# Kernel tuning notes

Measured on AMD Instinct MI355X. Metric: run time of the kernel, lower is better.

## Reference

```python
import jax, jax.numpy as jnp
import numpy as np

DIM = 512
EPS = 1e-8
LN_EPS = 1e-5


def _layernorm(x, g, b):
    mu = jnp.mean(x, axis=-1, keepdims=True)
    var = jnp.mean(jnp.square(x - mu), axis=-1, keepdims=True)
    return (x - mu) * jax.lax.rsqrt(var + LN_EPS) * g + b


def setup_inputs() -> dict:
    key = jax.random.key(0)
    ks = jax.random.split(key, 8)
    b, i, j, d = 8, 2048, 2048, DIM
    s = 1.0 / np.sqrt(d)
    return {
        "inputs": jax.random.normal(ks[0], (b, i, d), dtype=jnp.float32),
        "context": jax.random.normal(ks[1], (b, j, d), dtype=jnp.float32),
        "g_in": jnp.ones((d,), jnp.float32),
        "b_in": jnp.zeros((d,), jnp.float32),
        "g_ctx": jnp.ones((d,), jnp.float32),
        "b_ctx": jnp.zeros((d,), jnp.float32),
        "Wq": jax.random.uniform(ks[2], (d, d), jnp.float32, -s, s),
        "bq": jnp.zeros((d,), jnp.float32),
        "Wk": jax.random.uniform(ks[3], (d, d), jnp.float32, -s, s),
        "bk": jnp.zeros((d,), jnp.float32),
        "Wv": jax.random.uniform(ks[4], (d, d), jnp.float32, -s, s),
        "bv": jnp.zeros((d,), jnp.float32),
    }


def reference(inputs, context, g_in, b_in, g_ctx, b_ctx, Wq, bq, Wk, bk, Wv, bv):
    scale = DIM ** (-0.5)
    x = _layernorm(inputs, g_in, b_in)
    c = _layernorm(context, g_ctx, b_ctx)
    q = x @ Wq + bq          # [b,i,d]
    k = c @ Wk + bk          # [b,j,d]
    v = c @ Wv + bv          # [b,j,d]
    dots = jnp.einsum('bid,bjd->bij', q, k) * scale
    # NOTE: non-standard softmax over the QUERY axis (dim=1), then eps shift
    attn = jax.nn.softmax(dots, axis=1) + EPS
    # second renormalization over the KEY axis (dim=2)
    mean_attn = attn / (jnp.sum(attn, axis=2, keepdims=True) + EPS)
    updates = jnp.einsum('bjd,bij->bid', v, mean_attn)
    return updates
```

## Files before the change

kernel.cpp:

```cpp
#include <hip/hip_runtime.h>
#include <hip/hip_bf16.h>
#include <math.h>

#define EPSF 1e-8f
#define LN_EPSF 1e-5f
#define SCALE_QK 0.04419417382415922f

typedef unsigned short ushort_t;
typedef __bf16 bhalf;
typedef bhalf bhalf8 __attribute__((ext_vector_type(8)));
typedef float f32x4 __attribute__((ext_vector_type(4)));

__device__ __forceinline__ float b2f(ushort_t u) {
    return __uint_as_float((unsigned)u << 16);
}
__device__ __forceinline__ ushort_t f2b(float f) {
    unsigned x = __float_as_uint(f);
    return (ushort_t)((x + 0x7fffu + ((x >> 16) & 1u)) >> 16);
}
__device__ __forceinline__ unsigned mulpack2(unsigned u, float ca, float cb) {
    float lo = b2f((ushort_t)(u & 0xffffu)) * ca;
    float hi = b2f((ushort_t)(u >> 16)) * cb;
    return (unsigned)f2b(lo) | ((unsigned)f2b(hi) << 16);
}
__device__ __forceinline__ uint4 scale8(uint4 a, float4 c0, float4 c1) {
    a.x = mulpack2(a.x, c0.x, c0.y);
    a.y = mulpack2(a.y, c0.z, c0.w);
    a.z = mulpack2(a.z, c1.x, c1.y);
    a.w = mulpack2(a.w, c1.z, c1.w);
    return a;
}

__global__ __launch_bounds__(256) void ln_apply_kernel(
    const float* __restrict__ X1, const float* __restrict__ X2,
    const float* __restrict__ g1, const float* __restrict__ b1,
    const float* __restrict__ g2, const float* __restrict__ b2,
    ushort_t* __restrict__ O1, ushort_t* __restrict__ O2)
{
    const bool sec = blockIdx.y != 0;
    const float* X = sec ? X2 : X1;
    const float* g = sec ? g2 : g1;
    const float* b = sec ? b2 : b1;
    ushort_t* O = sec ? O2 : O1;
    const size_t base = (size_t)blockIdx.x * 512;
    const int t = threadIdx.x;
    float a = X[base + t];
    float c = X[base + t + 256];
    float s = a + c;
    float q = fmaf(a, a, c * c);
#pragma unroll
    for (int off = 32; off > 0; off >>= 1) {
        s += __shfl_down(s, off, 64);
        q += __shfl_down(q, off, 64);
    }
    __shared__ float ls[4], lq[4], mv[2];
    int lane = t & 63, w = t >> 6;
    if (lane == 0) { ls[w] = s; lq[w] = q; }
    __syncthreads();
    if (t == 0) {
        float st = ls[0] + ls[1] + ls[2] + ls[3];
        float qt = lq[0] + lq[1] + lq[2] + lq[3];
        float mu = st * (1.0f / 512.0f);
        float var = qt * (1.0f / 512.0f) - mu * mu;
        mv[0] = mu;
        mv[1] = rsqrtf(var + LN_EPSF);
    }
    __syncthreads();
    float mu = mv[0], rstd = mv[1];
    O[base + t]       = f2b((a - mu) * rstd * g[t] + b[t]);
    O[base + t + 256] = f2b((c - mu) * rstd * g[t + 256] + b[t + 256]);
}

__global__ __launch_bounds__(256) void wtrans_kernel(
    const float* __restrict__ W0, const float* __restrict__ W1,
    const float* __restrict__ W2,
    ushort_t* __restrict__ T0, ushort_t* __restrict__ T1,
    ushort_t* __restrict__ T2)
{
    const float* W = blockIdx.z == 0 ? W0 : (blockIdx.z == 1 ? W1 : W2);
    ushort_t* T = blockIdx.z == 0 ? T0 : (blockIdx.z == 1 ? T1 : T2);
    __shared__ float tile[32][33];
    int tx = threadIdx.x & 31, ty = threadIdx.x >> 5;
    int r0 = blockIdx.y * 32, c0 = blockIdx.x * 32;
#pragma unroll
    for (int p = 0; p < 4; ++p)
        tile[ty + p * 8][tx] = W[(size_t)(r0 + ty + p * 8) * 512 + c0 + tx];
    __syncthreads();
#pragma unroll
    for (int p = 0; p < 4; ++p)
        T[(size_t)(c0 + ty + p * 8) * 512 + r0 + tx] = f2b(tile[tx][ty + p * 8]);
}

__global__ __launch_bounds__(256) void vtrans_kernel(
    const ushort_t* __restrict__ V, ushort_t* __restrict__ VT)
{
    __shared__ ushort_t tile[32][33];
    const size_t vb = (size_t)blockIdx.z * 2048 * 512;
    const size_t tb = (size_t)blockIdx.z * 512 * 2048;
    int tx = threadIdx.x & 31, ty = threadIdx.x >> 5;
    int j0 = blockIdx.y * 32, d0 = blockIdx.x * 32;
#pragma unroll
    for (int p = 0; p < 4; ++p)
        tile[ty + p * 8][tx] = V[vb + (size_t)(j0 + ty + p * 8) * 512 + d0 + tx];
    __syncthreads();
#pragma unroll
    for (int p = 0; p < 4; ++p)
        VT[tb + (size_t)(d0 + ty + p * 8) * 2048 + j0 + tx] = tile[tx][ty + p * 8];
}

template <int MODE>
__global__ __launch_bounds__(256) void mfma_gemm_kernel(
    const ushort_t* __restrict__ A, const ushort_t* __restrict__ B,
    void* __restrict__ Cout, const float* __restrict__ aux,
    float* __restrict__ colsum, const float* __restrict__ colrecip,
    int K, int N, size_t strideA, size_t strideB, size_t strideC,
    int auxStride, float scale)
{
    __shared__ ushort_t As[128][40];
    __shared__ ushort_t Bs[128][40];
    const int tid = threadIdx.x;
    const ushort_t* Ab = A + strideA * blockIdx.z;
    const ushort_t* Bb = B + strideB * blockIdx.z;
    const int m0 = blockIdx.y * 128;
    const int n0 = blockIdx.x * 128;
    const int sr = tid >> 2;
    const int sc = (tid & 3) * 8;
    const int wave = tid >> 6;
    const int lane = tid & 63;
    const int fm = lane & 15;
    const int fq = lane >> 4;
    const int wm = (wave >> 1) * 64;
    const int wn = (wave & 1) * 64;

    f32x4 acc[4][4];
#pragma unroll
    for (int i = 0; i < 4; ++i)
#pragma unroll
        for (int j = 0; j < 4; ++j) acc[i][j] = (f32x4){0.f, 0.f, 0.f, 0.f};

    const ushort_t* Arow0 = Ab + (size_t)(m0 + sr) * K + sc;
    const ushort_t* Arow1 = Ab + (size_t)(m0 + sr + 64) * K + sc;
    const ushort_t* Brow0 = Bb + (size_t)(n0 + sr) * K + sc;
    const ushort_t* Brow1 = Bb + (size_t)(n0 + sr + 64) * K + sc;

    for (int k0 = 0; k0 < K; k0 += 32) {
        uint4 a0 = *(const uint4*)(Arow0 + k0);
        uint4 a1 = *(const uint4*)(Arow1 + k0);
        uint4 b0 = *(const uint4*)(Brow0 + k0);
        uint4 b1 = *(const uint4*)(Brow1 + k0);
        if (MODE == 2) {
            const float* cr = colrecip + 2048 * blockIdx.z + k0 + sc;
            float4 c0 = *(const float4*)cr;
            float4 c1 = *(const float4*)(cr + 4);
            a0 = scale8(a0, c0, c1);
            a1 = scale8(a1, c0, c1);
        }
        __syncthreads();
        *(uint4*)&As[sr][sc] = a0;
        *(uint4*)&As[sr + 64][sc] = a1;
        *(uint4*)&Bs[sr][sc] = b0;
        *(uint4*)&Bs[sr + 64][sc] = b1;
        __syncthreads();
        bhalf8 af[4], bfr[4];
#pragma unroll
        for (int t = 0; t < 4; ++t) {
            af[t]  = *(const bhalf8*)&As[wm + t * 16 + fm][fq * 8];
            bfr[t] = *(const bhalf8*)&Bs[wn + t * 16 + fm][fq * 8];
        }
#pragma unroll
        for (int i = 0; i < 4; ++i)
#pragma unroll
            for (int j = 0; j < 4; ++j)
                acc[i][j] = __builtin_amdgcn_mfma_f32_16x16x32_bf16(
                    af[i], bfr[j], acc[i][j], 0, 0, 0);
    }

    if (MODE == 2) {
        float* C = (float*)Cout + strideC * blockIdx.z;
        const float* rc = aux + (size_t)auxStride * blockIdx.z;
#pragma unroll
        for (int ti = 0; ti < 4; ++ti) {
#pragma unroll
            for (int r = 0; r < 4; ++r) {
                int row = m0 + wm + ti * 16 + fq * 4 + r;
                float rs = rc[row];
#pragma unroll
                for (int tj = 0; tj < 4; ++tj) {
                    int col = n0 + wn + tj * 16 + fm;
                    C[(size_t)row * N + col] = acc[ti][tj][r] * rs;
                }
            }
        }
    } else if (MODE == 1) {
        ushort_t* C = (ushort_t*)Cout + strideC * blockIdx.z;
        float* colpart = (float*)&As[0][0];
        __syncthreads();
        if (tid < 128) colpart[tid] = 0.f;
        __syncthreads();
        float psum[4] = {0.f, 0.f, 0.f, 0.f};
#pragma unroll
        for (int ti = 0; ti < 4; ++ti) {
#pragma unroll
            for (int r = 0; r < 4; ++r) {
                int row = m0 + wm + ti * 16 + fq * 4 + r;
#pragma unroll
                for (int tj = 0; tj < 4; ++tj) {
                    int col = n0 + wn + tj * 16 + fm;
                    float e = __expf(acc[ti][tj][r] * scale);
                    ushort_t h = f2b(e);
                    C[(size_t)row * N + col] = h;
                    psum[tj] += b2f(h);
                }
            }
        }
#pragma unroll
        for (int tj = 0; tj < 4; ++tj)
            atomicAdd(&colpart[wn + tj * 16 + fm], psum[tj]);
        __syncthreads();
        if (tid < 128)
            atomicAdd(&colsum[2048 * blockIdx.z + n0 + tid], colpart[tid]);
    } else {
        ushort_t* C = (ushort_t*)Cout + strideC * blockIdx.z;
#pragma unroll
        for (int ti = 0; ti < 4; ++ti) {
#pragma unroll
            for (int r = 0; r < 4; ++r) {
                int row = m0 + wm + ti * 16 + fq * 4 + r;
#pragma unroll
                for (int tj = 0; tj < 4; ++tj) {
                    int col = n0 + wn + tj * 16 + fm;
                    C[(size_t)row * N + col] = f2b(acc[ti][tj][r] + aux[col]);
                }
            }
        }
    }
}

__global__ __launch_bounds__(256) void colrecip_kernel(
    const float* __restrict__ cs, float* __restrict__ cr)
{
    int t = blockIdx.x * 256 + threadIdx.x;
    cr[t] = 1.0f / cs[t];
}

__global__ __launch_bounds__(256) void rowsum_kernel(
    const ushort_t* __restrict__ E, const float* __restrict__ colrecip,
    float* __restrict__ recip)
{
    const uint4* rp = (const uint4*)(E + (size_t)blockIdx.x * 2048);
    const float4* cr = (const float4*)(colrecip + (blockIdx.x >> 11) * 2048);
    uint4 u = rp[threadIdx.x];
    float4 c0 = cr[threadIdx.x * 2];
    float4 c1 = cr[threadIdx.x * 2 + 1];
    float s = b2f((ushort_t)(u.x & 0xffffu)) * c0.x
            + b2f((ushort_t)(u.x >> 16))    * c0.y
            + b2f((ushort_t)(u.y & 0xffffu)) * c0.z
            + b2f((ushort_t)(u.y >> 16))    * c0.w
            + b2f((ushort_t)(u.z & 0xffffu)) * c1.x
            + b2f((ushort_t)(u.z >> 16))    * c1.y
            + b2f((ushort_t)(u.w & 0xffffu)) * c1.z
            + b2f((ushort_t)(u.w >> 16))    * c1.w;
#pragma unroll
    for (int off = 32; off > 0; off >>= 1) s += __shfl_down(s, off, 64);
    __shared__ float ls[4];
    int lane = threadIdx.x & 63, wv = threadIdx.x >> 6;
    if (lane == 0) ls[wv] = s;
    __syncthreads();
    if (threadIdx.x == 0)
        recip[blockIdx.x] = 1.0f / (ls[0] + ls[1] + ls[2] + ls[3] + 2.049e-5f);
}

extern "C" void kernel_launch(void* const* d_in, const int* in_sizes, int n_in,
                              void* d_out, int out_size, void* d_ws, size_t ws_size,
                              hipStream_t stream)
{
    const float* inputs  = (const float*)d_in[0];
    const float* context = (const float*)d_in[1];
    const float* g_in    = (const float*)d_in[2];
    const float* b_in    = (const float*)d_in[3];
    const float* g_ctx   = (const float*)d_in[4];
    const float* b_ctx   = (const float*)d_in[5];
    const float* Wq      = (const float*)d_in[6];
    const float* bq      = (const float*)d_in[7];
    const float* Wk      = (const float*)d_in[8];
    const float* bk      = (const float*)d_in[9];
    const float* Wv      = (const float*)d_in[10];
    const float* bv      = (const float*)d_in[11];
    float* out = (float*)d_out;

    const size_t QKV  = 8ull * 2048 * 512;
    const size_t WSZ  = 512ull * 512;
    const size_t DOTS = 8ull * 2048 * 2048;

    ushort_t* xln   = (ushort_t*)d_ws;
    ushort_t* cln   = xln + QKV;
    ushort_t* WqT   = cln + QKV;
    ushort_t* WkT   = WqT + WSZ;
    ushort_t* WvT   = WkT + WSZ;
    ushort_t* q     = WvT + WSZ;
    ushort_t* kk    = q + QKV;
    ushort_t* v     = kk + QKV;
    ushort_t* vT    = v + QKV;
    ushort_t* edots = vT + QKV;
    float* recip    = (float*)(edots + DOTS);
    float* colsum   = recip + 16384;
    float* colrecip = colsum + 16384;
    size_t need_bytes = (6 * QKV + 3 * WSZ + DOTS) * 2 + 3 * 16384 * 4;
    if (ws_size < need_bytes) return;

    hipMemsetAsync(colsum, 0, 16384 * sizeof(float), stream);

    ln_apply_kernel<<<dim3(16384, 2), 256, 0, stream>>>(
        inputs, context, g_in, b_in, g_ctx, b_ctx, xln, cln);

    wtrans_kernel<<<dim3(16, 16, 3), 256, 0, stream>>>(Wq, Wk, Wv, WqT, WkT, WvT);

    mfma_gemm_kernel<0><<<dim3(4, 128, 1), 256, 0, stream>>>(
        xln, WqT, q, bq, nullptr, nullptr, 512, 512, 0, 0, 0, 0, 1.f);
    mfma_gemm_kernel<0><<<dim3(4, 128, 1), 256, 0, stream>>>(
        cln, WkT, kk, bk, nullptr, nullptr, 512, 512, 0, 0, 0, 0, 1.f);
    mfma_gemm_kernel<0><<<dim3(4, 128, 1), 256, 0, stream>>>(
        cln, WvT, v, bv, nullptr, nullptr, 512, 512, 0, 0, 0, 0, 1.f);

    vtrans_kernel<<<dim3(16, 64, 8), 256, 0, stream>>>(v, vT);

    mfma_gemm_kernel<1><<<dim3(16, 16, 8), 256, 0, stream>>>(
        q, kk, edots, nullptr, colsum, nullptr, 512, 2048,
        (size_t)2048 * 512, (size_t)2048 * 512, (size_t)2048 * 2048, 0, SCALE_QK);

    colrecip_kernel<<<64, 256, 0, stream>>>(colsum, colrecip);
    rowsum_kernel<<<16384, 256, 0, stream>>>(edots, colrecip, recip);

    mfma_gemm_kernel<2><<<dim3(4, 16, 8), 256, 0, stream>>>(
        edots, vT, out, recip, nullptr, colrecip, 2048, 512,
        (size_t)2048 * 2048, (size_t)512 * 2048, (size_t)2048 * 512, 2048, 1.f);
}
```

Measured before the change: 367.8 us.

## Use direct global-to-LDS loads with XOR swizzle and fold colrecip into V transpose

The GEMM main loop now fetches A/B tiles with global_load_lds straight into an XOR-swizzled LDS layout. The K step grows from 32 to 64, which halves the number of barriers. The per-column softmax reciprocal is moved out of the final GEMM's A-operand load and applied once when V is transposed. The column-sum epilogue reduces across lanes with shuffles before the LDS atomics. Together these aim to remove register staging, bank conflicts and repeated scaling work, at the cost of extra bf16 rounding on the scaled V instead of the scaled exp values.

```diff
diff --git a/kernel.cpp b/kernel.cpp
--- a/kernel.cpp
+++ b/kernel.cpp
@@ -18,17 +18,10 @@
     unsigned x = __float_as_uint(f);
     return (ushort_t)((x + 0x7fffu + ((x >> 16) & 1u)) >> 16);
 }
-__device__ __forceinline__ unsigned mulpack2(unsigned u, float ca, float cb) {
-    float lo = b2f((ushort_t)(u & 0xffffu)) * ca;
-    float hi = b2f((ushort_t)(u >> 16)) * cb;
-    return (unsigned)f2b(lo) | ((unsigned)f2b(hi) << 16);
-}
-__device__ __forceinline__ uint4 scale8(uint4 a, float4 c0, float4 c1) {
-    a.x = mulpack2(a.x, c0.x, c0.y);
-    a.y = mulpack2(a.y, c0.z, c0.w);
-    a.z = mulpack2(a.z, c1.x, c1.y);
-    a.w = mulpack2(a.w, c1.z, c1.w);
-    return a;
+__device__ __forceinline__ void gload16(const ushort_t* g, ushort_t* l) {
+    __builtin_amdgcn_global_load_lds(
+        (const __attribute__((address_space(1))) unsigned int*)g,
+        (__attribute__((address_space(3))) unsigned int*)l, 16, 0, 0);
 }
 
 __global__ __launch_bounds__(256) void ln_apply_kernel(
@@ -91,8 +84,9 @@
         T[(size_t)(c0 + ty + p * 8) * 512 + r0 + tx] = f2b(tile[tx][ty + p * 8]);
 }
 
-__global__ __launch_bounds__(256) void vtrans_kernel(
-    const ushort_t* __restrict__ V, ushort_t* __restrict__ VT)
+__global__ __launch_bounds__(256) void vtrans_scaled_kernel(
+    const ushort_t* __restrict__ V, const float* __restrict__ colrecip,
+    ushort_t* __restrict__ VT)
 {
     __shared__ ushort_t tile[32][33];
     const size_t vb = (size_t)blockIdx.z * 2048 * 512;
@@ -102,77 +96,90 @@
 #pragma unroll
     for (int p = 0; p < 4; ++p)
         tile[ty + p * 8][tx] = V[vb + (size_t)(j0 + ty + p * 8) * 512 + d0 + tx];
+    float cr = colrecip[blockIdx.z * 2048 + j0 + tx];
     __syncthreads();
 #pragma unroll
     for (int p = 0; p < 4; ++p)
-        VT[tb + (size_t)(d0 + ty + p * 8) * 2048 + j0 + tx] = tile[tx][ty + p * 8];
+        VT[tb + (size_t)(d0 + ty + p * 8) * 2048 + j0 + tx] =
+            f2b(b2f(tile[tx][ty + p * 8]) * cr);
 }
 
 template <int MODE>
 __global__ __launch_bounds__(256) void mfma_gemm_kernel(
     const ushort_t* __restrict__ A, const ushort_t* __restrict__ B,
     void* __restrict__ Cout, const float* __restrict__ aux,
-    float* __restrict__ colsum, const float* __restrict__ colrecip,
+    float* __restrict__ colsum,
     int K, int N, size_t strideA, size_t strideB, size_t strideC,
     int auxStride, float scale)
 {
-    __shared__ ushort_t As[128][40];
-    __shared__ ushort_t Bs[128][40];
+    __shared__ __align__(16) ushort_t As[128 * 64];
+    __shared__ __align__(16) ushort_t Bs[128 * 64];
     const int tid = threadIdx.x;
     const ushort_t* Ab = A + strideA * blockIdx.z;
     const ushort_t* Bb = B + strideB * blockIdx.z;
     const int m0 = blockIdx.y * 128;
     const int n0 = blockIdx.x * 128;
-    const int sr = tid >> 2;
-    const int sc = (tid & 3) * 8;
     const int wave = tid >> 6;
     const int lane = tid & 63;
     const int fm = lane & 15;
     const int fq = lane >> 4;
+    const int fm7 = fm & 7;
     const int wm = (wave >> 1) * 64;
     const int wn = (wave & 1) * 64;
 
+    const int lrow = lane >> 3;
+    const int lchunk = lane & 7;
+    const int scs = lchunk ^ lrow;
+
+    const ushort_t* aSrc[4]; const ushort_t* bSrc[4];
+    ushort_t* aDst[4]; ushort_t* bDst[4];
+#pragma unroll
+    for (int p = 0; p < 4; ++p) {
+        int row = wave * 32 + p * 8 + lrow;
+        aSrc[p] = Ab + (size_t)(m0 + row) * K + scs * 8;
+        bSrc[p] = Bb + (size_t)(n0 + row) * K + scs * 8;
+        aDst[p] = As + (wave * 32 + p * 8) * 64 + lane * 8;
+        bDst[p] = Bs + (wave * 32 + p * 8) * 64 + lane * 8;
+    }
+
+    const int cBase = fq ^ fm7;
+    const ushort_t* aFrag[4]; const ushort_t* bFrag[4];
+#pragma unroll
+    for (int t = 0; t < 4; ++t) {
+        aFrag[t] = As + (wm + t * 16 + fm) * 64;
+        bFrag[t] = Bs + (wn + t * 16 + fm) * 64;
+    }
+
     f32x4 acc[4][4];
 #pragma unroll
     for (int i = 0; i < 4; ++i)
 #pragma unroll
         for (int j = 0; j < 4; ++j) acc[i][j] = (f32x4){0.f, 0.f, 0.f, 0.f};
 
-    const ushort_t* Arow0 = Ab + (size_t)(m0 + sr) * K + sc;
-    const ushort_t* Arow1 = Ab + (size_t)(m0 + sr + 64) * K + sc;
-    const ushort_t* Brow0 = Bb + (size_t)(n0 + sr) * K + sc;
-    const ushort_t* Brow1 = Bb + (size_t)(n0 + sr + 64) * K + sc;
-
-    for (int k0 = 0; k0 < K; k0 += 32) {
-        uint4 a0 = *(const uint4*)(Arow0 + k0);
-        uint4 a1 = *(const uint4*)(Arow1 + k0);
-        uint4 b0 = *(const uint4*)(Brow0 + k0);
-        uint4 b1 = *(const uint4*)(Brow1 + k0);
-        if (MODE == 2) {
-            const float* cr = colrecip + 2048 * blockIdx.z + k0 + sc;
-            float4 c0 = *(const float4*)cr;
-            float4 c1 = *(const float4*)(cr + 4);
-            a0 = scale8(a0, c0, c1);
-            a1 = scale8(a1, c0, c1);
-        }
-        __syncthreads();
-        *(uint4*)&As[sr][sc] = a0;
-        *(uint4*)&As[sr + 64][sc] = a1;
-        *(uint4*)&Bs[sr][sc] = b0;
-        *(uint4*)&Bs[sr + 64][sc] = b1;
-        __syncthreads();
-        bhalf8 af[4], bfr[4];
-#pragma unroll
-        for (int t = 0; t < 4; ++t) {
-            af[t]  = *(const bhalf8*)&As[wm + t * 16 + fm][fq * 8];
-            bfr[t] = *(const bhalf8*)&Bs[wn + t * 16 + fm][fq * 8];
-        }
-#pragma unroll
-        for (int i = 0; i < 4; ++i)
-#pragma unroll
-            for (int j = 0; j < 4; ++j)
-                acc[i][j] = __builtin_amdgcn_mfma_f32_16x16x32_bf16(
-                    af[i], bfr[j], acc[i][j], 0, 0, 0);
+    for (int k0 = 0; k0 < K; k0 += 64) {
+        __syncthreads();
+#pragma unroll
+        for (int p = 0; p < 4; ++p) {
+            gload16(aSrc[p] + k0, aDst[p]);
+            gload16(bSrc[p] + k0, bDst[p]);
+        }
+        __syncthreads();
+#pragma unroll
+        for (int s = 0; s < 2; ++s) {
+            const int off = ((cBase ^ (s << 2)) << 3);
+            bhalf8 af[4], bf[4];
+#pragma unroll
+            for (int t = 0; t < 4; ++t) {
+                af[t] = *(const bhalf8*)(aFrag[t] + off);
+                bf[t] = *(const bhalf8*)(bFrag[t] + off);
+            }
+#pragma unroll
+            for (int i = 0; i < 4; ++i)
+#pragma unroll
+                for (int j = 0; j < 4; ++j)
+                    acc[i][j] = __builtin_amdgcn_mfma_f32_16x16x32_bf16(
+                        af[i], bf[j], acc[i][j], 0, 0, 0);
+        }
     }
 
     if (MODE == 2) {
@@ -193,10 +200,7 @@
         }
     } else if (MODE == 1) {
         ushort_t* C = (ushort_t*)Cout + strideC * blockIdx.z;
-        float* colpart = (float*)&As[0][0];
-        __syncthreads();
-        if (tid < 128) colpart[tid] = 0.f;
-        __syncthreads();
+        float* colpart = (float*)&As[0];
         float psum[4] = {0.f, 0.f, 0.f, 0.f};
 #pragma unroll
         for (int ti = 0; ti < 4; ++ti) {
@@ -214,8 +218,18 @@
             }
         }
 #pragma unroll
-        for (int tj = 0; tj < 4; ++tj)
-            atomicAdd(&colpart[wn + tj * 16 + fm], psum[tj]);
+        for (int tj = 0; tj < 4; ++tj) {
+            psum[tj] += __shfl_xor(psum[tj], 16, 64);
+            psum[tj] += __shfl_xor(psum[tj], 32, 64);
+        }
+        __syncthreads();
+        if (tid < 128) colpart[tid] = 0.f;
+        __syncthreads();
+        if (fq == 0) {
+#pragma unroll
+            for (int tj = 0; tj < 4; ++tj)
+                atomicAdd(&colpart[wn + tj * 16 + fm], psum[tj]);
+        }
         __syncthreads();
         if (tid < 128)
             atomicAdd(&colsum[2048 * blockIdx.z + n0 + tid], colpart[tid]);
@@ -300,8 +314,8 @@
     ushort_t* q     = WvT + WSZ;
     ushort_t* kk    = q + QKV;
     ushort_t* v     = kk + QKV;
-    ushort_t* vT    = v + QKV;
-    ushort_t* edots = vT + QKV;
+    ushort_t* vTs   = v + QKV;
+    ushort_t* edots = vTs + QKV;
     float* recip    = (float*)(edots + DOTS);
     float* colsum   = recip + 16384;
     float* colrecip = colsum + 16384;
@@ -316,22 +330,23 @@
     wtrans_kernel<<<dim3(16, 16, 3), 256, 0, stream>>>(Wq, Wk, Wv, WqT, WkT, WvT);
 
     mfma_gemm_kernel<0><<<dim3(4, 128, 1), 256, 0, stream>>>(
-        xln, WqT, q, bq, nullptr, nullptr, 512, 512, 0, 0, 0, 0, 1.f);
+        xln, WqT, q, bq, nullptr, 512, 512, 0, 0, 0, 0, 1.f);
     mfma_gemm_kernel<0><<<dim3(4, 128, 1), 256, 0, stream>>>(
-        cln, WkT, kk, bk, nullptr, nullptr, 512, 512, 0, 0, 0, 0, 1.f);
+        cln, WkT, kk, bk, nullptr, 512, 512, 0, 0, 0, 0, 1.f);
     mfma_gemm_kernel<0><<<dim3(4, 128, 1), 256, 0, stream>>>(
-        cln, WvT, v, bv, nullptr, nullptr, 512, 512, 0, 0, 0, 0, 1.f);
-
-    vtrans_kernel<<<dim3(16, 64, 8), 256, 0, stream>>>(v, vT);
+        cln, WvT, v, bv, nullptr, 512, 512, 0, 0, 0, 0, 1.f);
 
     mfma_gemm_kernel<1><<<dim3(16, 16, 8), 256, 0, stream>>>(
-        q, kk, edots, nullptr, colsum, nullptr, 512, 2048,
+        q, kk, edots, nullptr, colsum, 512, 2048,
         (size_t)2048 * 512, (size_t)2048 * 512, (size_t)2048 * 2048, 0, SCALE_QK);
 
     colrecip_kernel<<<64, 256, 0, stream>>>(colsum, colrecip);
+
+    vtrans_scaled_kernel<<<dim3(16, 64, 8), 256, 0, stream>>>(v, colrecip, vTs);
+
     rowsum_kernel<<<16384, 256, 0, stream>>>(edots, colrecip, recip);
 
     mfma_gemm_kernel<2><<<dim3(4, 16, 8), 256, 0, stream>>>(
-        edots, vT, out, recip, nullptr, colrecip, 2048, 512,
+        edots, vTs, out, recip, nullptr, 2048, 512,
         (size_t)2048 * 2048, (size_t)512 * 2048, (size_t)2048 * 512, 2048, 1.f);
 }
```

Result: faster. 317.1 us (-13.8%).
